# Optimization experiments

Measured on AMD Instinct MI355X. Metric: run time of the kernel, lower is better.

## Reference

```python
import jax, jax.numpy as jnp
import numpy as np

N, C, H, W = 32, 256, 56, 56
LN_EPS = 1e-5


def make_dct_filters(c, h, w):
    # Multi-spectral DCT pooling filters (FcaNet-style), bnumfre=4 frequency pairs,
    # channels split into 4 equal groups. DctCFea source unavailable; this is the
    # standard implementation pattern for such a module.
    freqs = [(0, 0), (0, 1), (1, 0), (1, 1)]
    cpf = c // len(freqs)
    f = np.zeros((c, h, w), np.float32)
    for i, (u, v) in enumerate(freqs):
        bh = np.cos(np.pi * u * (np.arange(h) + 0.5) / h) / np.sqrt(h)
        if u != 0:
            bh = bh * np.sqrt(2.0)
        bw = np.cos(np.pi * v * (np.arange(w) + 0.5) / w) / np.sqrt(w)
        if v != 0:
            bw = bw * np.sqrt(2.0)
        f[i * cpf:(i + 1) * cpf] = (bh[:, None] * bw[None, :]).astype(np.float32)
    return jnp.asarray(f)


DCT_F = make_dct_filters(C, H, W)  # (C,H,W) constant buffer


def _ln(s, g, b):
    # LayerNorm over the channel dim (normalized_shape [C,1] / [C,1,1] -> stats over C)
    mu = s.mean(axis=1, keepdims=True)
    var = ((s - mu) ** 2).mean(axis=1, keepdims=True)
    return (s - mu) * jax.lax.rsqrt(var + LN_EPS) * g + b


def setup_inputs() -> dict:
    key = jax.random.key(0)
    ks = jax.random.split(key, 8)
    return {
        "x": jax.random.normal(ks[0], (N, C, H, W), dtype=jnp.float32),
        "gc_w": jax.random.normal(ks[1], (C,), dtype=jnp.float32) * 0.02,
        "gc_b": jnp.zeros((), dtype=jnp.float32),
        "lc_w": jax.random.normal(ks[2], (3,), dtype=jnp.float32) * 0.3,
        "lc_b": jnp.zeros((), dtype=jnp.float32),
        "lcln_g": jnp.ones((C,), dtype=jnp.float32),
        "lcln_b": jnp.zeros((C,), dtype=jnp.float32),
        "tw_w": jax.random.normal(ks[3], (C, C), dtype=jnp.float32) * 0.02,
        "tw_b": jnp.zeros((C,), dtype=jnp.float32),
        "twln_g": jnp.ones((C,), dtype=jnp.float32),
        "twln_b": jnp.zeros((C,), dtype=jnp.float32),
        "wdct": jnp.full((C,), 0.5, dtype=jnp.float32),
        "wmax": jnp.full((C,), 0.5, dtype=jnp.float32),
    }


def reference(x, gc_w, gc_b, lc_w, lc_b, lcln_g, lcln_b, tw_w, tw_b, twln_g, twln_b, wdct, wmax):
    n, c, h, w = x.shape
    xf = x.reshape(n, c, h * w)                                   # (N,C,HW)
    # global context: 1x1 conv to 1 channel, softmax over space, weighted spatial sum
    logits = jnp.einsum('ncs,c->ns', xf, gc_w) + gc_b             # (N,HW)
    attn = jax.nn.softmax(logits, axis=-1)
    x_g = jnp.einsum('ncs,ns->nc', xf, attn)                      # (N,C)
    # pooled stats: max pool + DCT multi-spectral pool, learned blend
    x_max = xf.max(axis=-1)                                       # (N,C)
    x_dct = jnp.einsum('nchw,chw->nc', x, DCT_F)                  # (N,C)
    x_s = wmax * x_max + wdct * x_dct                             # (N,C)
    # local conv1d (k=3, pad=1) across the channel axis
    p = jnp.pad(x_s, ((0, 0), (1, 1)))
    x_l = lc_w[0] * p[:, :-2] + lc_w[1] * p[:, 1:-1] + lc_w[2] * p[:, 2:] + lc_b
    # LayerNorm over channels, 1x1 transform, LayerNorm, sigmoid gate
    att = _ln(x_g + x_s + x_l, lcln_g, lcln_b)                    # (N,C)
    att = att @ tw_w.T + tw_b                                     # tw: 1x1 conv C->C
    gate = jax.nn.sigmoid(_ln(att, twln_g, twln_b))               # (N,C)
    return x * gate[:, :, None, None]
```

## Files before the change

### kernel.cpp

```cpp
#include <hip/hip_runtime.h>
#include <math.h>


#define N_ 32
#define C_ 256
#define H_ 56
#define W_ 56
#define S_ 3136
#define LN_EPS 1e-5f

__device__ __forceinline__ float wave_sum(float v) {
  #pragma unroll
  for (int o = 32; o > 0; o >>= 1) v += __shfl_xor(v, o);
  return v;
}
__device__ __forceinline__ float wave_max(float v) {
  #pragma unroll
  for (int o = 32; o > 0; o >>= 1) v = fmaxf(v, __shfl_xor(v, o));
  return v;
}
__device__ __forceinline__ float block_sum(float v, float* red) {
  int lane = threadIdx.x & 63, wid = threadIdx.x >> 6;
  float w = wave_sum(v);
  __syncthreads();
  if (lane == 0) red[wid] = w;
  __syncthreads();
  return red[0] + red[1] + red[2] + red[3];
}

__global__ void k_logits(const float* __restrict__ x, const float* __restrict__ gc_w,
                         float* __restrict__ logits) {
  __shared__ float gw[C_];
  int tid = threadIdx.x;
  gw[tid] = gc_w[tid];
  __syncthreads();
  int n = blockIdx.y;
  int s = blockIdx.x * 256 + tid;
  if (s >= S_) return;
  const float* xp = x + (size_t)n * C_ * S_ + s;
  float acc = 0.f;
  #pragma unroll 8
  for (int c = 0; c < C_; ++c) acc += xp[(size_t)c * S_] * gw[c];
  logits[n * S_ + s] = acc;
}

__global__ void k_softmax(const float* __restrict__ logits, float* __restrict__ attn) {
  int n = blockIdx.x, tid = threadIdx.x;
  __shared__ float red[4];
  float v[13];
  float m = -INFINITY;
  #pragma unroll
  for (int k = 0; k < 13; ++k) {
    int s = tid + k * 256;
    v[k] = (s < S_) ? logits[n * S_ + s] : -INFINITY;
    m = fmaxf(m, v[k]);
  }
  float wm = wave_max(m);
  int lane = tid & 63, wid = tid >> 6;
  if (lane == 0) red[wid] = wm;
  __syncthreads();
  m = fmaxf(fmaxf(red[0], red[1]), fmaxf(red[2], red[3]));
  float z = 0.f;
  #pragma unroll
  for (int k = 0; k < 13; ++k) { v[k] = expf(v[k] - m); z += v[k]; }
  z = block_sum(z, red);
  float inv = 1.f / z;
  #pragma unroll
  for (int k = 0; k < 13; ++k) {
    int s = tid + k * 256;
    if (s < S_) attn[n * S_ + s] = v[k] * inv;
  }
}

__global__ void k_stats(const float* __restrict__ x, const float* __restrict__ attn,
                        float* __restrict__ xg, float* __restrict__ xmax,
                        float* __restrict__ xdct) {
  int c = blockIdx.x, n = blockIdx.y;
  int tid = threadIdx.x;
  __shared__ float bh[H_], bw[W_];
  __shared__ float red[3][4];
  int grp = c >> 6;
  int u = grp >> 1, v = grp & 1;
  const float invs = 0.13363062f;
  const float sq2  = 1.41421356f;
  if (tid < H_) {
    float b = cosf((float)M_PI * u * (tid + 0.5f) / H_) * invs;
    bh[tid] = u ? b * sq2 : b;
  } else if (tid < H_ + W_) {
    int w = tid - H_;
    float b = cosf((float)M_PI * v * (w + 0.5f) / W_) * invs;
    bw[w] = v ? b * sq2 : b;
  }
  __syncthreads();
  const float* xp = x + ((size_t)n * C_ + c) * S_;
  const float* ap = attn + n * S_;
  float g = 0.f, mx = -INFINITY, d = 0.f;
  for (int s = tid; s < S_; s += 256) {
    float xv = xp[s];
    g += xv * ap[s];
    mx = fmaxf(mx, xv);
    int h = s / W_;
    d += xv * bh[h] * bw[s - h * W_];
  }
  float gs = wave_sum(g), ms = wave_max(mx), ds = wave_sum(d);
  int lane = tid & 63, wid = tid >> 6;
  if (lane == 0) { red[0][wid] = gs; red[1][wid] = ms; red[2][wid] = ds; }
  __syncthreads();
  if (tid == 0) {
    xg[n * C_ + c]   = red[0][0] + red[0][1] + red[0][2] + red[0][3];
    xmax[n * C_ + c] = fmaxf(fmaxf(red[1][0], red[1][1]), fmaxf(red[1][2], red[1][3]));
    xdct[n * C_ + c] = red[2][0] + red[2][1] + red[2][2] + red[2][3];
  }
}

__global__ void k_gate(const float* __restrict__ xg, const float* __restrict__ xmax,
                       const float* __restrict__ xdct,
                       const float* __restrict__ lc_w, const float* __restrict__ lc_b,
                       const float* __restrict__ lcln_g, const float* __restrict__ lcln_b,
                       const float* __restrict__ tw_w, const float* __restrict__ tw_b,
                       const float* __restrict__ twln_g, const float* __restrict__ twln_b,
                       const float* __restrict__ wdct, const float* __restrict__ wmax,
                       float* __restrict__ gate) {
  int n = blockIdx.x, c = threadIdx.x;
  __shared__ float xs[C_ + 2];
  __shared__ float att_s[C_];
  __shared__ float red[4];
  float g  = xg[n * C_ + c];
  float sv = wmax[c] * xmax[n * C_ + c] + wdct[c] * xdct[n * C_ + c];
  xs[c + 1] = sv;
  if (c == 0) { xs[0] = 0.f; xs[C_ + 1] = 0.f; }
  __syncthreads();
  float xl = lc_w[0] * xs[c] + lc_w[1] * xs[c + 1] + lc_w[2] * xs[c + 2] + lc_b[0];
  float t = g + sv + xl;
  float mu  = block_sum(t, red) * (1.f / C_);
  float dv  = t - mu;
  float var = block_sum(dv * dv, red) * (1.f / C_);
  float att = dv * rsqrtf(var + LN_EPS) * lcln_g[c] + lcln_b[c];
  att_s[c] = att;
  __syncthreads();
  float a2 = tw_b[c];
  const float4* wrow = (const float4*)(tw_w + c * C_);
  const float4* arow = (const float4*)att_s;
  #pragma unroll 8
  for (int k = 0; k < C_ / 4; ++k) {
    float4 wv = wrow[k], av = arow[k];
    a2 += wv.x * av.x + wv.y * av.y + wv.z * av.z + wv.w * av.w;
  }
  float mu2  = block_sum(a2, red) * (1.f / C_);
  float d2   = a2 - mu2;
  float var2 = block_sum(d2 * d2, red) * (1.f / C_);
  float z = d2 * rsqrtf(var2 + LN_EPS) * twln_g[c] + twln_b[c];
  gate[n * C_ + c] = 1.f / (1.f + expf(-z));
}

__global__ void k_scale(const float* __restrict__ x, const float* __restrict__ gate,
                        float* __restrict__ out) {
  const float4* x4 = (const float4*)x;
  float4* o4 = (float4*)out;
  const int total = N_ * C_ * (S_ / 4);
  for (int i = blockIdx.x * blockDim.x + threadIdx.x; i < total;
       i += gridDim.x * blockDim.x) {
    int nc = i / (S_ / 4);
    float gv = gate[nc];
    float4 v = x4[i];
    v.x *= gv; v.y *= gv; v.z *= gv; v.w *= gv;
    o4[i] = v;
  }
}

extern "C" void kernel_launch(void* const* d_in, const int* in_sizes, int n_in,
                              void* d_out, int out_size, void* d_ws, size_t ws_size,
                              hipStream_t stream) {
  const float* x      = (const float*)d_in[0];
  const float* gc_w   = (const float*)d_in[1];
  const float* lc_w   = (const float*)d_in[3];
  const float* lc_b   = (const float*)d_in[4];
  const float* lcln_g = (const float*)d_in[5];
  const float* lcln_b = (const float*)d_in[6];
  const float* tw_w   = (const float*)d_in[7];
  const float* tw_b   = (const float*)d_in[8];
  const float* twln_g = (const float*)d_in[9];
  const float* twln_b = (const float*)d_in[10];
  const float* wdct   = (const float*)d_in[11];
  const float* wmax   = (const float*)d_in[12];
  float* out = (float*)d_out;

  float* ws     = (float*)d_ws;
  float* logits = ws;
  float* attn   = ws + (size_t)N_ * S_;
  float* xg     = ws + (size_t)2 * N_ * S_;
  float* xmax_  = xg + N_ * C_;
  float* xdct_  = xmax_ + N_ * C_;
  float* gate   = xdct_ + N_ * C_;

  hipLaunchKernelGGL(k_logits, dim3((S_ + 255) / 256, N_), dim3(256), 0, stream,
                     x, gc_w, logits);
  hipLaunchKernelGGL(k_softmax, dim3(N_), dim3(256), 0, stream, logits, attn);
  hipLaunchKernelGGL(k_stats, dim3(C_, N_), dim3(256), 0, stream,
                     x, attn, xg, xmax_, xdct_);
  hipLaunchKernelGGL(k_gate, dim3(N_), dim3(256), 0, stream,
                     xg, xmax_, xdct_, lc_w, lc_b, lcln_g, lcln_b,
                     tw_w, tw_b, twln_g, twln_b, wdct, wmax, gate);
  hipLaunchKernelGGL(k_scale, dim3(2048), dim3(256), 0, stream, x, gate, out);
}
```

Baseline: 92.37 us.

## Split logits over channel chunks, vectorize stats loads, nontemporal output stores

The logits kernel now splits the channel reduction into 32 chunks of 8 channels, one block per chunk and batch element. It writes partial logits to workspace, and the softmax kernel sums them, which gives far more blocks and float4-coalesced loads. The stats kernel switches to float4 loads and precomputes the DCT width basis as float4, which removes the per-element division. The scale kernel uses nontemporal stores for the output. In exchange, softmax has to read 32x more partial data from workspace, and the workspace grows accordingly.

```diff
diff --git a/kernel.cpp b/kernel.cpp
--- a/kernel.cpp
+++ b/kernel.cpp
@@ -7,7 +7,13 @@
 #define H_ 56
 #define W_ 56
 #define S_ 3136
+#define Q_ 784
 #define LN_EPS 1e-5f
+
+#define NCH 32
+#define CPC 8
+
+using f4 = __attribute__((ext_vector_type(4))) float;
 
 __device__ __forceinline__ float wave_sum(float v) {
   #pragma unroll
@@ -27,24 +33,33 @@
   __syncthreads();
   return red[0] + red[1] + red[2] + red[3];
 }
+__device__ __forceinline__ float dot4(f4 a, f4 b) {
+  return a.x * b.x + a.y * b.y + a.z * b.z + a.w * b.w;
+}
 
 __global__ void k_logits(const float* __restrict__ x, const float* __restrict__ gc_w,
-                         float* __restrict__ logits) {
-  __shared__ float gw[C_];
-  int tid = threadIdx.x;
-  gw[tid] = gc_w[tid];
-  __syncthreads();
-  int n = blockIdx.y;
-  int s = blockIdx.x * 256 + tid;
-  if (s >= S_) return;
-  const float* xp = x + (size_t)n * C_ * S_ + s;
-  float acc = 0.f;
-  #pragma unroll 8
-  for (int c = 0; c < C_; ++c) acc += xp[(size_t)c * S_] * gw[c];
-  logits[n * S_ + s] = acc;
-}
-
-__global__ void k_softmax(const float* __restrict__ logits, float* __restrict__ attn) {
+                         float* __restrict__ lpart) {
+  int n = blockIdx.y, ch = blockIdx.x, tid = threadIdx.x;
+  int c0 = ch * CPC;
+  __shared__ float gw[CPC];
+  if (tid < CPC) gw[tid] = gc_w[c0 + tid];
+  __syncthreads();
+  const f4* xb = (const f4*)(x + ((size_t)n * C_ + c0) * S_);
+  f4 a0 = {0,0,0,0}, a1 = {0,0,0,0}, a2 = {0,0,0,0}, a3 = {0,0,0,0};
+  #pragma unroll
+  for (int c = 0; c < CPC; ++c) {
+    const f4* xp = xb + (size_t)c * Q_;
+    float w = gw[c];
+    f4 v0 = xp[tid], v1 = xp[tid + 256], v2 = xp[tid + 512];
+    a0 += w * v0; a1 += w * v1; a2 += w * v2;
+    if (tid < 16) { f4 v3 = xp[768 + tid]; a3 += w * v3; }
+  }
+  f4* lp = (f4*)(lpart + ((size_t)ch * N_ + n) * S_);
+  lp[tid] = a0; lp[tid + 256] = a1; lp[tid + 512] = a2;
+  if (tid < 16) lp[768 + tid] = a3;
+}
+
+__global__ void k_softmax(const float* __restrict__ lpart, float* __restrict__ attn) {
   int n = blockIdx.x, tid = threadIdx.x;
   __shared__ float red[4];
   float v[13];
@@ -52,8 +67,15 @@
   #pragma unroll
   for (int k = 0; k < 13; ++k) {
     int s = tid + k * 256;
-    v[k] = (s < S_) ? logits[n * S_ + s] : -INFINITY;
-    m = fmaxf(m, v[k]);
+    float acc = -INFINITY;
+    if (s < S_) {
+      acc = 0.f;
+      #pragma unroll 8
+      for (int ch = 0; ch < NCH; ++ch)
+        acc += lpart[((size_t)ch * N_ + n) * S_ + s];
+    }
+    v[k] = acc;
+    m = fmaxf(m, acc);
   }
   float wm = wave_max(m);
   int lane = tid & 63, wid = tid >> 6;
@@ -75,32 +97,47 @@
 __global__ void k_stats(const float* __restrict__ x, const float* __restrict__ attn,
                         float* __restrict__ xg, float* __restrict__ xmax,
                         float* __restrict__ xdct) {
-  int c = blockIdx.x, n = blockIdx.y;
-  int tid = threadIdx.x;
-  __shared__ float bh[H_], bw[W_];
+  int c = blockIdx.x, n = blockIdx.y, tid = threadIdx.x;
+  __shared__ float bh[H_];
+  __shared__ f4 bw4[14];
   __shared__ float red[3][4];
   int grp = c >> 6;
-  int u = grp >> 1, v = grp & 1;
+  int u = grp >> 1, vv = grp & 1;
   const float invs = 0.13363062f;
   const float sq2  = 1.41421356f;
   if (tid < H_) {
     float b = cosf((float)M_PI * u * (tid + 0.5f) / H_) * invs;
     bh[tid] = u ? b * sq2 : b;
-  } else if (tid < H_ + W_) {
-    int w = tid - H_;
-    float b = cosf((float)M_PI * v * (w + 0.5f) / W_) * invs;
-    bw[w] = v ? b * sq2 : b;
-  }
-  __syncthreads();
-  const float* xp = x + ((size_t)n * C_ + c) * S_;
-  const float* ap = attn + n * S_;
-  float g = 0.f, mx = -INFINITY, d = 0.f;
-  for (int s = tid; s < S_; s += 256) {
-    float xv = xp[s];
-    g += xv * ap[s];
-    mx = fmaxf(mx, xv);
-    int h = s / W_;
-    d += xv * bh[h] * bw[s - h * W_];
+  } else if (tid >= 64 && tid < 64 + 14) {
+    int j = tid - 64;
+    f4 b;
+    #pragma unroll
+    for (int e = 0; e < 4; ++e) {
+      float t = cosf((float)M_PI * vv * (4 * j + e + 0.5f) / W_) * invs;
+      ((float*)&b)[e] = vv ? t * sq2 : t;
+    }
+    bw4[j] = b;
+  }
+  __syncthreads();
+  const f4* xp = (const f4*)(x + ((size_t)n * C_ + c) * S_);
+  const f4* ap = (const f4*)(attn + (size_t)n * S_);
+  float g = 0.f, d = 0.f, mx = -INFINITY;
+  #pragma unroll
+  for (int k = 0; k < 3; ++k) {
+    int q = tid + k * 256;
+    f4 xv = xp[q], av = ap[q];
+    g += dot4(xv, av);
+    mx = fmaxf(fmaxf(fmaxf(xv.x, xv.y), fmaxf(xv.z, xv.w)), mx);
+    int h = q / 14;
+    d += bh[h] * dot4(xv, bw4[q - h * 14]);
+  }
+  if (tid < 16) {
+    int q = 768 + tid;
+    f4 xv = xp[q], av = ap[q];
+    g += dot4(xv, av);
+    mx = fmaxf(fmaxf(fmaxf(xv.x, xv.y), fmaxf(xv.z, xv.w)), mx);
+    int h = q / 14;
+    d += bh[h] * dot4(xv, bw4[q - h * 14]);
   }
   float gs = wave_sum(g), ms = wave_max(mx), ds = wave_sum(d);
   int lane = tid & 63, wid = tid >> 6;
@@ -139,13 +176,10 @@
   att_s[c] = att;
   __syncthreads();
   float a2 = tw_b[c];
-  const float4* wrow = (const float4*)(tw_w + c * C_);
-  const float4* arow = (const float4*)att_s;
+  const f4* wrow = (const f4*)(tw_w + c * C_);
+  const f4* arow = (const f4*)att_s;
   #pragma unroll 8
-  for (int k = 0; k < C_ / 4; ++k) {
-    float4 wv = wrow[k], av = arow[k];
-    a2 += wv.x * av.x + wv.y * av.y + wv.z * av.z + wv.w * av.w;
-  }
+  for (int k = 0; k < C_ / 4; ++k) a2 += dot4(wrow[k], arow[k]);
   float mu2  = block_sum(a2, red) * (1.f / C_);
   float d2   = a2 - mu2;
   float var2 = block_sum(d2 * d2, red) * (1.f / C_);
@@ -155,16 +189,16 @@
 
 __global__ void k_scale(const float* __restrict__ x, const float* __restrict__ gate,
                         float* __restrict__ out) {
-  const float4* x4 = (const float4*)x;
-  float4* o4 = (float4*)out;
-  const int total = N_ * C_ * (S_ / 4);
+  const f4* x4 = (const f4*)x;
+  f4* o4 = (f4*)out;
+  const int total = N_ * C_ * Q_;
   for (int i = blockIdx.x * blockDim.x + threadIdx.x; i < total;
        i += gridDim.x * blockDim.x) {
-    int nc = i / (S_ / 4);
+    int nc = i / Q_;
     float gv = gate[nc];
-    float4 v = x4[i];
-    v.x *= gv; v.y *= gv; v.z *= gv; v.w *= gv;
-    o4[i] = v;
+    f4 v = x4[i];
+    v *= gv;
+    __builtin_nontemporal_store(v, &o4[i]);
   }
 }
 
@@ -185,19 +219,17 @@
   const float* wmax   = (const float*)d_in[12];
   float* out = (float*)d_out;
 
-  float* ws     = (float*)d_ws;
-  float* logits = ws;
-  float* attn   = ws + (size_t)N_ * S_;
-  float* xg     = ws + (size_t)2 * N_ * S_;
-  float* xmax_  = xg + N_ * C_;
-  float* xdct_  = xmax_ + N_ * C_;
-  float* gate   = xdct_ + N_ * C_;
-
-  hipLaunchKernelGGL(k_logits, dim3((S_ + 255) / 256, N_), dim3(256), 0, stream,
-                     x, gc_w, logits);
-  hipLaunchKernelGGL(k_softmax, dim3(N_), dim3(256), 0, stream, logits, attn);
-  hipLaunchKernelGGL(k_stats, dim3(C_, N_), dim3(256), 0, stream,
-                     x, attn, xg, xmax_, xdct_);
+  float* ws    = (float*)d_ws;
+  float* lpart = ws;
+  float* attn  = lpart + (size_t)NCH * N_ * S_;
+  float* xg    = attn + (size_t)N_ * S_;
+  float* xmax_ = xg + N_ * C_;
+  float* xdct_ = xmax_ + N_ * C_;
+  float* gate  = xdct_ + N_ * C_;
+
+  hipLaunchKernelGGL(k_logits, dim3(NCH, N_), dim3(256), 0, stream, x, gc_w, lpart);
+  hipLaunchKernelGGL(k_softmax, dim3(N_), dim3(256), 0, stream, lpart, attn);
+  hipLaunchKernelGGL(k_stats, dim3(C_, N_), dim3(256), 0, stream, x, attn, xg, xmax_, xdct_);
   hipLaunchKernelGGL(k_gate, dim3(N_), dim3(256), 0, stream,
                      xg, xmax_, xdct_, lc_w, lc_b, lcln_g, lcln_b,
                      tw_w, tw_b, twln_g, twln_b, wdct, wmax, gate);
```

New measurement: 115.1 us. 1.25x slower.
